# Performance work log

Measured on AMD Instinct MI355X. Metric: run time of the kernel, lower is better.

## Reference

```python
import math
import jax, jax.numpy as jnp
import numpy as np

D = 1024      # d_model
H = 16        # n_heads
HD = 64       # head_dim
DKV = D // 2  # 512
KVHD = DKV // H  # 32
HID = D // 8  # 128 (tau/delta hidden)
B, L, F = 2, 2048, 32


def setup_inputs() -> dict:
    key = jax.random.key(0)
    ks = jax.random.split(key, 16)
    s = 0.02
    return {
        "h": jax.random.normal(ks[0], (B, L, D), jnp.float32),
        "pre_norm_mu": jax.random.normal(ks[1], (B, L, F), jnp.float32),
        "pre_norm_sigma": jax.random.uniform(ks[2], (B, L, F), jnp.float32),
        "Wq": jax.random.normal(ks[3], (D, D), jnp.float32) * s,
        "Wk": jax.random.normal(ks[4], (D, DKV), jnp.float32) * s,
        "Wv": jax.random.normal(ks[5], (D, DKV), jnp.float32) * s,
        "Wo": jax.random.normal(ks[6], (DKV, D), jnp.float32) * s,
        "bo": jnp.zeros((D,), jnp.float32),
        "tau_w1": jax.random.normal(ks[7], (D + 1, HID), jnp.float32) * s,
        "tau_b1": jnp.zeros((HID,), jnp.float32),
        "tau_w2": jax.random.normal(ks[8], (HID, 1), jnp.float32) * s,
        "tau_b2": jnp.zeros((1,), jnp.float32),
        "del_w1": jax.random.normal(ks[9], (D + 1, HID), jnp.float32) * s,
        "del_b1": jnp.zeros((HID,), jnp.float32),
        "del_w2": jax.random.normal(ks[10], (HID, DKV), jnp.float32) * s,
        "del_b2": jnp.zeros((DKV,), jnp.float32),
    }


def _mlp(x, w1, b1, w2, b2):
    # Linear -> exact GELU -> Linear (matches torch nn.GELU default)
    return jax.nn.gelu(x @ w1 + b1, approximate=False) @ w2 + b2


def reference(h, pre_norm_mu, pre_norm_sigma, Wq, Wk, Wv, Wo, bo,
              tau_w1, tau_b1, tau_w2, tau_b2, del_w1, del_b1, del_w2, del_b2):
    b, l, _ = h.shape
    sigma_mean = jnp.clip(pre_norm_sigma.mean(axis=-1, keepdims=True), 1e-6, None)  # (B,L,1)
    mu_mean = pre_norm_mu.mean(axis=-1, keepdims=True)                               # (B,L,1)

    tau = jnp.exp(jnp.clip(_mlp(jnp.concatenate([sigma_mean, h], -1),
                                tau_w1, tau_b1, tau_w2, tau_b2), -3.0, 3.0))  # (B,L,1)
    delta = jnp.clip(_mlp(jnp.concatenate([mu_mean, h], -1),
                          del_w1, del_b1, del_w2, del_b2), -5.0, 5.0)          # (B,L,DKV)

    Q = (h @ Wq).reshape(b, l, H, HD).transpose(0, 2, 1, 3)       # (B,H,L,HD)
    K = (h @ Wk).reshape(b, l, H, KVHD).transpose(0, 2, 1, 3)     # (B,H,L,KVHD)
    V = (h @ Wv).reshape(b, l, H, KVHD).transpose(0, 2, 1, 3)

    Qc = Q[..., :KVHD]                                            # (B,H,L,KVHD)
    logits = jnp.einsum('bhqd,bhkd->bhqk', Qc, K) / math.sqrt(KVHD)
    logits = tau[:, None] * logits                                # tau -> (B,1,L,1): per-query scale

    delta_r = delta.reshape(b, l, H, KVHD).transpose(0, 2, 1, 3)  # (B,H,L,KVHD)
    delta_last = delta_r[:, :, -1, :]                             # (B,H,KVHD)
    delta_bias = jnp.einsum('bhd,bhkd->bhk', delta_last, K)       # (B,H,L_k)
    logits = logits + delta_bias[:, :, None, :]

    logits = jnp.clip(logits, -50.0, 50.0)
    causal = jnp.triu(jnp.ones((l, l), bool), 1)
    logits = jnp.where(causal, -jnp.inf, logits)

    attn = jax.nn.softmax(logits, axis=-1)
    out = jnp.einsum('bhqk,bhkd->bhqd', attn, V)                  # (B,H,L,KVHD)
    out = out.transpose(0, 2, 1, 3).reshape(b, l, DKV)
    out = out @ Wo + bo
    return out[:, -1, :]                                          # (B,D)
```

## Files before the change

### kernel.cpp

```cpp
#include <hip/hip_runtime.h>
#include <hip/hip_bf16.h>

#define Dm   1024
#define Hh   16
#define HDq  64
#define DKV  512
#define HID  128
#define Bb   2
#define Ll   2048
#define Ff   32

typedef _Float16 half8 __attribute__((ext_vector_type(8)));
typedef float f32x4 __attribute__((ext_vector_type(4)));

__device__ __forceinline__ float gelu_exact(float x) {
    return 0.5f * x * (1.0f + erff(x * 0.70710678118654752f));
}

__global__ __launch_bounds__(256) void kpart(
        const float* __restrict__ h, const float* __restrict__ Wq,
        const float* __restrict__ tw1, const float* __restrict__ dw1,
        float* __restrict__ hid_part, float* __restrict__ qc_part)
{
    const int bx = blockIdx.x, t = threadIdx.x;
    __shared__ float hl[128];
    __shared__ float red[256];
    if (bx < 32) {
        const int id = bx;
        const int b = (id >> 4) & 1, which = (id >> 3) & 1, jsplit = id & 7;
        const float* w1 = which ? dw1 : tw1;
        const float* hrow = h + ((size_t)b * Ll + (Ll - 1)) * Dm + jsplit * 128;
        if (t < 128) hl[t] = hrow[t];
        __syncthreads();
        const int col = t & 127, rg = t >> 7;
        const float* w1p = w1 + (size_t)(jsplit * 128 + rg + 1) * HID + col;
        float acc = 0.f;
#pragma unroll 8
        for (int p = 0; p < 64; ++p)
            acc += hl[p * 2 + rg] * w1p[(size_t)p * 2 * HID];
        red[t] = acc;
        __syncthreads();
        if (t < 128)
            hid_part[(((size_t)(b * 2 + which)) * 8 + jsplit) * HID + t] = red[t] + red[t + 128];
    } else {
        const int id = bx - 32;
        const int b = id >> 3, jsplit = id & 7;
        const float* hrow = h + ((size_t)b * Ll + (Ll - 1)) * Dm + jsplit * 128;
        if (t < 128) hl[t] = hrow[t];
        __syncthreads();
        const int c0 = t, c1 = t + 256;
        const int colq0 = (c0 >> 5) * HDq + (c0 & 31);
        const int colq1 = (c1 >> 5) * HDq + (c1 & 31);
        const float* Wq0 = Wq + (size_t)(jsplit * 128) * Dm;
        float a0 = 0.f, a1 = 0.f;
#pragma unroll 8
        for (int j = 0; j < 128; ++j) {
            const float x = hl[j];
            a0 += x * Wq0[(size_t)j * Dm + colq0];
            a1 += x * Wq0[(size_t)j * Dm + colq1];
        }
        float* qp = qc_part + ((size_t)b * 8 + jsplit) * DKV;
        qp[c0] = a0;
        qp[c1] = a1;
    }
}

__global__ __launch_bounds__(256) void kwcomb(
        const float* __restrict__ mu, const float* __restrict__ sigma,
        const float* __restrict__ tw1, const float* __restrict__ tb1,
        const float* __restrict__ tw2, const float* __restrict__ tb2,
        const float* __restrict__ dw1, const float* __restrict__ db1,
        const float* __restrict__ dw2, const float* __restrict__ db2,
        const float* __restrict__ hid_part, const float* __restrict__ qc_part,
        float* __restrict__ w_comb)
{
    const int cs = blockIdx.x, b = blockIdx.y;
    const int t = threadIdx.x;
    __shared__ float gh[HID];
    __shared__ float red[256];
    __shared__ float s_tau, s_sm, s_mm;

    if (t == 0) {
        float s = 0.f;
        for (int f = 0; f < Ff; ++f) s += sigma[((size_t)b * Ll + (Ll - 1)) * Ff + f];
        s_sm = fmaxf(s / (float)Ff, 1e-6f);
    }
    if (t == 64) {
        float s = 0.f;
        for (int f = 0; f < Ff; ++f) s += mu[((size_t)b * Ll + (Ll - 1)) * Ff + f];
        s_mm = s / (float)Ff;
    }
    __syncthreads();

    if (t < 128) {
        float a = tb1[t] + s_sm * tw1[t];
#pragma unroll
        for (int s = 0; s < 8; ++s)
            a += hid_part[(((size_t)(b * 2 + 0)) * 8 + s) * HID + t];
        red[t] = gelu_exact(a) * tw2[t];
    } else {
        const int hh = t - 128;
        float a = db1[hh] + s_mm * dw1[hh];
#pragma unroll
        for (int s = 0; s < 8; ++s)
            a += hid_part[(((size_t)(b * 2 + 1)) * 8 + s) * HID + hh];
        gh[hh] = gelu_exact(a);
        red[t] = 0.f;
    }
    __syncthreads();
    for (int s = 128; s > 0; s >>= 1) {
        if (t < s) red[t] += red[t + s];
        __syncthreads();
    }
    if (t == 0) {
        float s = red[0] + tb2[0];
        s_tau = expf(fminf(fmaxf(s, -3.f), 3.f));
    }
    __syncthreads();

    const int cl = t & 63, ih = t >> 6;
    const int c = cs * 64 + cl;
    float dacc = 0.f;
#pragma unroll 8
    for (int i = ih * 32; i < ih * 32 + 32; ++i)
        dacc += gh[i] * dw2[(size_t)i * DKV + c];
    red[t] = dacc;
    __syncthreads();
    if (t < 64) {
        const int cc = cs * 64 + t;
        float d = red[t] + red[t + 64] + red[t + 128] + red[t + 192] + db2[cc];
        d = fminf(fmaxf(d, -5.f), 5.f);
        float q = 0.f;
#pragma unroll
        for (int s = 0; s < 8; ++s)
            q += qc_part[((size_t)b * 8 + s) * DKV + cc];
        w_comb[(size_t)b * DKV + cc] = s_tau * q * 0.17677669529663687f + d;
    }
}

__global__ __launch_bounds__(256) void kkw(
        const float* __restrict__ Wk, const float* __restrict__ w_comb,
        _Float16* __restrict__ kwh16)
{
    const int jt = blockIdx.x, b = blockIdx.y;
    const int t = threadIdx.x;
    __shared__ float wc[DKV];
    __shared__ float kl[16][36];
    {
        float2 v = *(const float2*)(w_comb + (size_t)b * DKV + t * 2);
        wc[t * 2] = v.x; wc[t * 2 + 1] = v.y;
    }
    __syncthreads();
    const int c0 = t * 2;
    const float w0 = wc[c0], w1 = wc[c0 + 1];
    const int hd = t >> 4;
#pragma unroll 4
    for (int jj = 0; jj < 32; ++jj) {
        const int j = jt * 32 + jj;
        float2 kv = *(const float2*)(Wk + (size_t)j * DKV + c0);
        float p = kv.x * w0 + kv.y * w1;
        p += __shfl_xor(p, 1); p += __shfl_xor(p, 2);
        p += __shfl_xor(p, 4); p += __shfl_xor(p, 8);
        if ((t & 15) == 0) kl[hd][jj] = p;
    }
    __syncthreads();
    if (t < 64) {
        const int head = t & 15, jl = (t >> 4) * 8;
        half8 v;
#pragma unroll
        for (int e = 0; e < 8; ++e) v[e] = (_Float16)kl[head][jl + e];
        *(half8*)(kwh16 + ((size_t)(b * 32 + jt)) * 512 + t * 8) = v;
    }
}

__global__ __launch_bounds__(256) void klogit(
        const float* __restrict__ h, const _Float16* __restrict__ kwh16,
        float* __restrict__ p_arr, float* __restrict__ den_part)
{
    __shared__ __align__(16) _Float16 Kw[16384];
    __shared__ float lred[4][16][16];
    __shared__ float pden[16][16];
    const int bx = blockIdx.x, t = threadIdx.x;
    const int w = t >> 6, l = t & 63;
    const int rows0 = bx * 16, b = bx >> 7;

#pragma unroll
    for (int i = 0; i < 8; ++i) {
        const int idx = i * 256 + t;
        *(half8*)(Kw + idx * 8) = *(const half8*)(kwh16 + (size_t)b * 16384 + idx * 8);
    }
    __syncthreads();

    f32x4 lacc = {};
    const float* ap = h + (size_t)(rows0 + (l & 15)) * Dm + (l >> 4) * 8;
#pragma unroll
    for (int kk = 0; kk < 8; ++kk) {
        const int kt = w * 8 + kk;
        float4 x0 = *(const float4*)(ap + kt * 32);
        float4 x1 = *(const float4*)(ap + kt * 32 + 4);
        half8 af;
        af[0] = (_Float16)x0.x; af[1] = (_Float16)x0.y; af[2] = (_Float16)x0.z; af[3] = (_Float16)x0.w;
        af[4] = (_Float16)x1.x; af[5] = (_Float16)x1.y; af[6] = (_Float16)x1.z; af[7] = (_Float16)x1.w;
        half8 kf = *(const half8*)(Kw + kt * 512 + l * 8);
        lacc = __builtin_amdgcn_mfma_f32_16x16x32_f16(af, kf, lacc, 0, 0, 0);
    }
#pragma unroll
    for (int r = 0; r < 4; ++r)
        lred[w][(l >> 4) * 4 + r][l & 15] = lacc[r];
    __syncthreads();

    const int row16 = t >> 4, head = t & 15;
    float val = lred[0][row16][head] + lred[1][row16][head]
              + lred[2][row16][head] + lred[3][row16][head];
    val = fminf(fmaxf(val, -50.f), 50.f);
    const float e = __expf(val - 50.f);
    p_arr[(size_t)(rows0 + row16) * 16 + head] = e;
    pden[row16][head] = e;
    __syncthreads();
    if (t < 16) {
        float s = 0.f;
#pragma unroll
        for (int r = 0; r < 16; ++r) s += pden[r][t];
        den_part[((size_t)b * 16 + t) * 128 + (bx & 127)] = s;
    }
}

__global__ __launch_bounds__(256) void khbar(
        const float* __restrict__ hmat, const float* __restrict__ p_arr,
        float* __restrict__ hbar_part)
{
    const int jt = blockIdx.x, ls = blockIdx.y, b = blockIdx.z;
    const int t = threadIdx.x;
    __shared__ float P[2048];
#pragma unroll
    for (int i = 0; i < 2; ++i) {
        const int idx = i * 256 + t;
        *(float4*)(P + idx * 4) =
            *(const float4*)(p_arr + ((size_t)(b * Ll + ls * 128)) * 16 + idx * 4);
    }
    __syncthreads();
    const int hd = t & 15, jq = t >> 4;
    const float* hp = hmat + ((size_t)(b * Ll + ls * 128)) * Dm + jt * 128 + jq * 8;
    float4 a0 = {0.f, 0.f, 0.f, 0.f}, a1 = {0.f, 0.f, 0.f, 0.f};
#pragma unroll 4
    for (int l = 0; l < 128; ++l) {
        const float p = P[l * 16 + hd];
        float4 v0 = *(const float4*)(hp + (size_t)l * Dm);
        float4 v1 = *(const float4*)(hp + (size_t)l * Dm + 4);
        a0.x += p * v0.x; a0.y += p * v0.y; a0.z += p * v0.z; a0.w += p * v0.w;
        a1.x += p * v1.x; a1.y += p * v1.y; a1.z += p * v1.z; a1.w += p * v1.w;
    }
    float* dst = hbar_part + (((size_t)(b * 16 + hd)) * 16 + ls) * Dm + jt * 128 + jq * 8;
    *(float4*)dst = a0;
    *(float4*)(dst + 4) = a1;
}

__global__ __launch_bounds__(256) void kopre(
        const float* __restrict__ hbar_part, const float* __restrict__ den_part,
        const float* __restrict__ Wv, float* __restrict__ opre)
{
    const int hd = blockIdx.x, b = blockIdx.y;
    const int t = threadIdx.x;
    __shared__ float hb[Dm];
    __shared__ float4 red4[256];
    __shared__ float dred[128];
    __shared__ float s_den;

    if (t < 128) dred[t] = den_part[((size_t)b * 16 + hd) * 128 + t];
    float4 a = {0.f, 0.f, 0.f, 0.f};
#pragma unroll
    for (int ls = 0; ls < 16; ++ls) {
        float4 v = *(const float4*)(hbar_part + (((size_t)(b * 16 + hd)) * 16 + ls) * Dm + t * 4);
        a.x += v.x; a.y += v.y; a.z += v.z; a.w += v.w;
    }
    *(float4*)(hb + t * 4) = a;
    __syncthreads();
    if (t < 64) dred[t] += dred[t + 64];
    __syncthreads();
    if (t < 32) dred[t] += dred[t + 32];
    __syncthreads();
    if (t == 0) {
        float s = 0.f;
        for (int i = 0; i < 32; ++i) s += dred[i];
        s_den = s;
    }
    __syncthreads();

    const int d4 = (t & 7) * 4, jq = t >> 3;
    float4 acc = {0.f, 0.f, 0.f, 0.f};
#pragma unroll 8
    for (int j = jq * 32; j < jq * 32 + 32; ++j) {
        const float x = hb[j];
        float4 wv = *(const float4*)(Wv + (size_t)j * DKV + hd * 32 + d4);
        acc.x += x * wv.x; acc.y += x * wv.y; acc.z += x * wv.z; acc.w += x * wv.w;
    }
    red4[t] = acc;
    __syncthreads();
    if (t < 8) {
        float4 s = {0.f, 0.f, 0.f, 0.f};
#pragma unroll
        for (int g = 0; g < 32; ++g) {
            float4 v = red4[g * 8 + t];
            s.x += v.x; s.y += v.y; s.z += v.z; s.w += v.w;
        }
        const float inv = 1.0f / s_den;
        s.x *= inv; s.y *= inv; s.z *= inv; s.w *= inv;
        *(float4*)(opre + ((size_t)b * Hh + hd) * 32 + t * 4) = s;
    }
}

__global__ __launch_bounds__(256) void kout(
        const float* __restrict__ opre, const float* __restrict__ Wo,
        const float* __restrict__ bo, float* __restrict__ out)
{
    const int nt = blockIdx.x, b = blockIdx.y;
    const int t = threadIdx.x;
    __shared__ float op[DKV];
    __shared__ float red[256];
    if (t < 128)
        *(float4*)(op + t * 4) = *(const float4*)(opre + (size_t)b * DKV + t * 4);
    __syncthreads();
    const int nl = t & 63, cg = t >> 6;
    const int n = nt * 64 + nl;
    float acc = 0.f;
#pragma unroll 8
    for (int c = cg * 128; c < cg * 128 + 128; ++c)
        acc += op[c] * Wo[(size_t)c * Dm + n];
    red[t] = acc;
    __syncthreads();
    if (t < 64)
        out[(size_t)b * Dm + n] = bo[n] + red[t] + red[t + 64] + red[t + 128] + red[t + 192];
}

extern "C" void kernel_launch(void* const* d_in, const int* in_sizes, int n_in,
                              void* d_out, int out_size, void* d_ws, size_t ws_size,
                              hipStream_t stream) {
    const float* h      = (const float*)d_in[0];
    const float* mu     = (const float*)d_in[1];
    const float* sigma  = (const float*)d_in[2];
    const float* Wq     = (const float*)d_in[3];
    const float* Wk     = (const float*)d_in[4];
    const float* Wv     = (const float*)d_in[5];
    const float* Wo     = (const float*)d_in[6];
    const float* bo     = (const float*)d_in[7];
    const float* tau_w1 = (const float*)d_in[8];
    const float* tau_b1 = (const float*)d_in[9];
    const float* tau_w2 = (const float*)d_in[10];
    const float* tau_b2 = (const float*)d_in[11];
    const float* del_w1 = (const float*)d_in[12];
    const float* del_b1 = (const float*)d_in[13];
    const float* del_w2 = (const float*)d_in[14];
    const float* del_b2 = (const float*)d_in[15];
    float* out = (float*)d_out;

    _Float16* kwh16  = (_Float16*)d_ws;
    float* p_arr     = (float*)(kwh16 + 32768);
    float* den_part  = p_arr + 65536;
    float* hid_part  = den_part + 4096;
    float* qc_part   = hid_part + 4096;
    float* w_comb    = qc_part + 8192;
    float* hbar_part = w_comb + 1024;
    float* opre      = hbar_part + 524288;

    kpart<<<48, 256, 0, stream>>>(h, Wq, tau_w1, del_w1, hid_part, qc_part);
    kwcomb<<<dim3(8, Bb), 256, 0, stream>>>(mu, sigma, tau_w1, tau_b1, tau_w2, tau_b2,
                                            del_w1, del_b1, del_w2, del_b2,
                                            hid_part, qc_part, w_comb);
    kkw<<<dim3(32, Bb), 256, 0, stream>>>(Wk, w_comb, kwh16);
    klogit<<<256, 256, 0, stream>>>(h, kwh16, p_arr, den_part);
    khbar<<<dim3(8, 16, Bb), 256, 0, stream>>>(h, p_arr, hbar_part);
    kopre<<<dim3(16, Bb), 256, 0, stream>>>(hbar_part, den_part, Wv, opre);
    kout<<<dim3(16, Bb), 256, 0, stream>>>(opre, Wo, bo, out);
}
```

Measured before the change: 62.88 us.

## Fuse kernel chain: merge wcomb into kkw and logits into hbar accumulation

Merges the delta/tau combine kernel into the Wk projection kernel, so each of the 64 blocks recomputes the small MLP tail redundantly instead of paying a separate launch. It also fuses the logit/exp kernel with the weighted h-sum kernel using 32-row tiles, which keeps probabilities in LDS and drops the p_arr global round-trip, and it vectorises the Wq load in kpart. Risks: the redundant MLP work across blocks, only 128 blocks in the fused mid kernel, and h being read twice within a block.

```diff
diff --git a/kernel.cpp b/kernel.cpp
--- a/kernel.cpp
+++ b/kernel.cpp
@@ -48,36 +48,39 @@
         const float* hrow = h + ((size_t)b * Ll + (Ll - 1)) * Dm + jsplit * 128;
         if (t < 128) hl[t] = hrow[t];
         __syncthreads();
-        const int c0 = t, c1 = t + 256;
-        const int colq0 = (c0 >> 5) * HDq + (c0 & 31);
-        const int colq1 = (c1 >> 5) * HDq + (c1 & 31);
-        const float* Wq0 = Wq + (size_t)(jsplit * 128) * Dm;
-        float a0 = 0.f, a1 = 0.f;
+        float4 acc = {0.f, 0.f, 0.f, 0.f};
+        const float* Wq0 = Wq + (size_t)(jsplit * 128) * Dm + t * 4;
 #pragma unroll 8
         for (int j = 0; j < 128; ++j) {
             const float x = hl[j];
-            a0 += x * Wq0[(size_t)j * Dm + colq0];
-            a1 += x * Wq0[(size_t)j * Dm + colq1];
+            float4 wq = *(const float4*)(Wq0 + (size_t)j * Dm);
+            acc.x += x * wq.x; acc.y += x * wq.y;
+            acc.z += x * wq.z; acc.w += x * wq.w;
         }
-        float* qp = qc_part + ((size_t)b * 8 + jsplit) * DKV;
-        qp[c0] = a0;
-        qp[c1] = a1;
-    }
-}
-
-__global__ __launch_bounds__(256) void kwcomb(
+        const int col = t * 4;
+        if ((col & 63) < 32) {
+            const int c = (col >> 6) * 32 + (col & 31);
+            *(float4*)(qc_part + ((size_t)b * 8 + jsplit) * DKV + c) = acc;
+        }
+    }
+}
+
+__global__ __launch_bounds__(256) void kkw2(
         const float* __restrict__ mu, const float* __restrict__ sigma,
         const float* __restrict__ tw1, const float* __restrict__ tb1,
         const float* __restrict__ tw2, const float* __restrict__ tb2,
         const float* __restrict__ dw1, const float* __restrict__ db1,
         const float* __restrict__ dw2, const float* __restrict__ db2,
+        const float* __restrict__ Wk,
         const float* __restrict__ hid_part, const float* __restrict__ qc_part,
-        float* __restrict__ w_comb)
-{
-    const int cs = blockIdx.x, b = blockIdx.y;
+        _Float16* __restrict__ kwh16)
+{
+    const int jt = blockIdx.x, b = blockIdx.y;
     const int t = threadIdx.x;
     __shared__ float gh[HID];
     __shared__ float red[256];
+    __shared__ float wc[DKV];
+    __shared__ float kl[16][36];
     __shared__ float s_tau, s_sm, s_mm;
 
     if (t == 0) {
@@ -118,46 +121,34 @@
     }
     __syncthreads();
 
-    const int cl = t & 63, ih = t >> 6;
-    const int c = cs * 64 + cl;
-    float dacc = 0.f;
-#pragma unroll 8
-    for (int i = ih * 32; i < ih * 32 + 32; ++i)
-        dacc += gh[i] * dw2[(size_t)i * DKV + c];
-    red[t] = dacc;
-    __syncthreads();
-    if (t < 64) {
-        const int cc = cs * 64 + t;
-        float d = red[t] + red[t + 64] + red[t + 128] + red[t + 192] + db2[cc];
-        d = fminf(fmaxf(d, -5.f), 5.f);
-        float q = 0.f;
-#pragma unroll
-        for (int s = 0; s < 8; ++s)
-            q += qc_part[((size_t)b * 8 + s) * DKV + cc];
-        w_comb[(size_t)b * DKV + cc] = s_tau * q * 0.17677669529663687f + d;
-    }
-}
-
-__global__ __launch_bounds__(256) void kkw(
-        const float* __restrict__ Wk, const float* __restrict__ w_comb,
-        _Float16* __restrict__ kwh16)
-{
-    const int jt = blockIdx.x, b = blockIdx.y;
-    const int t = threadIdx.x;
-    __shared__ float wc[DKV];
-    __shared__ float kl[16][36];
-    {
-        float2 v = *(const float2*)(w_comb + (size_t)b * DKV + t * 2);
-        wc[t * 2] = v.x; wc[t * 2 + 1] = v.y;
-    }
-    __syncthreads();
-    const int c0 = t * 2;
-    const float w0 = wc[c0], w1 = wc[c0 + 1];
+    const int c0 = t, c1 = t + 256;
+    float d0 = db2[c0], d1 = db2[c1];
+#pragma unroll 8
+    for (int i = 0; i < HID; ++i) {
+        const float x = gh[i];
+        d0 += x * dw2[(size_t)i * DKV + c0];
+        d1 += x * dw2[(size_t)i * DKV + c1];
+    }
+    d0 = fminf(fmaxf(d0, -5.f), 5.f);
+    d1 = fminf(fmaxf(d1, -5.f), 5.f);
+    float q0 = 0.f, q1 = 0.f;
+#pragma unroll
+    for (int s = 0; s < 8; ++s) {
+        const float* qp = qc_part + ((size_t)b * 8 + s) * DKV;
+        q0 += qp[c0];
+        q1 += qp[c1];
+    }
+    const float inv_sqrt = 0.17677669529663687f;
+    wc[c0] = s_tau * q0 * inv_sqrt + d0;
+    wc[c1] = s_tau * q1 * inv_sqrt + d1;
+    __syncthreads();
+
+    const float w0 = wc[t * 2], w1 = wc[t * 2 + 1];
     const int hd = t >> 4;
 #pragma unroll 4
     for (int jj = 0; jj < 32; ++jj) {
         const int j = jt * 32 + jj;
-        float2 kv = *(const float2*)(Wk + (size_t)j * DKV + c0);
+        float2 kv = *(const float2*)(Wk + (size_t)j * DKV + t * 2);
         float p = kv.x * w0 + kv.y * w1;
         p += __shfl_xor(p, 1); p += __shfl_xor(p, 2);
         p += __shfl_xor(p, 4); p += __shfl_xor(p, 8);
@@ -173,16 +164,17 @@
     }
 }
 
-__global__ __launch_bounds__(256) void klogit(
+__global__ __launch_bounds__(256) void kmid(
         const float* __restrict__ h, const _Float16* __restrict__ kwh16,
-        float* __restrict__ p_arr, float* __restrict__ den_part)
+        float* __restrict__ den_part, float* __restrict__ hbar_part)
 {
     __shared__ __align__(16) _Float16 Kw[16384];
-    __shared__ float lred[4][16][16];
-    __shared__ float pden[16][16];
-    const int bx = blockIdx.x, t = threadIdx.x;
+    __shared__ float lred[4][32][17];
+    __shared__ float p_lds[32][16];
+    const int rt = blockIdx.x, b = blockIdx.y;
+    const int t = threadIdx.x;
     const int w = t >> 6, l = t & 63;
-    const int rows0 = bx * 16, b = bx >> 7;
+    const int rows0 = (b * 64 + rt) * 32;
 
 #pragma unroll
     for (int i = 0; i < 8; ++i) {
@@ -191,68 +183,69 @@
     }
     __syncthreads();
 
-    f32x4 lacc = {};
+    f32x4 lacc[2] = {};
     const float* ap = h + (size_t)(rows0 + (l & 15)) * Dm + (l >> 4) * 8;
 #pragma unroll
-    for (int kk = 0; kk < 8; ++kk) {
-        const int kt = w * 8 + kk;
-        float4 x0 = *(const float4*)(ap + kt * 32);
-        float4 x1 = *(const float4*)(ap + kt * 32 + 4);
-        half8 af;
-        af[0] = (_Float16)x0.x; af[1] = (_Float16)x0.y; af[2] = (_Float16)x0.z; af[3] = (_Float16)x0.w;
-        af[4] = (_Float16)x1.x; af[5] = (_Float16)x1.y; af[6] = (_Float16)x1.z; af[7] = (_Float16)x1.w;
-        half8 kf = *(const half8*)(Kw + kt * 512 + l * 8);
-        lacc = __builtin_amdgcn_mfma_f32_16x16x32_f16(af, kf, lacc, 0, 0, 0);
-    }
-#pragma unroll
-    for (int r = 0; r < 4; ++r)
-        lred[w][(l >> 4) * 4 + r][l & 15] = lacc[r];
-    __syncthreads();
-
-    const int row16 = t >> 4, head = t & 15;
-    float val = lred[0][row16][head] + lred[1][row16][head]
-              + lred[2][row16][head] + lred[3][row16][head];
-    val = fminf(fmaxf(val, -50.f), 50.f);
-    const float e = __expf(val - 50.f);
-    p_arr[(size_t)(rows0 + row16) * 16 + head] = e;
-    pden[row16][head] = e;
-    __syncthreads();
+    for (int mt = 0; mt < 2; ++mt) {
+        const float* apm = ap + (size_t)mt * 16 * Dm;
+#pragma unroll
+        for (int ks = 0; ks < 8; ++ks) {
+            const int kt = w * 8 + ks;
+            float4 x0 = *(const float4*)(apm + kt * 32);
+            float4 x1 = *(const float4*)(apm + kt * 32 + 4);
+            half8 af;
+            af[0] = (_Float16)x0.x; af[1] = (_Float16)x0.y; af[2] = (_Float16)x0.z; af[3] = (_Float16)x0.w;
+            af[4] = (_Float16)x1.x; af[5] = (_Float16)x1.y; af[6] = (_Float16)x1.z; af[7] = (_Float16)x1.w;
+            half8 kf = *(const half8*)(Kw + kt * 512 + l * 8);
+            lacc[mt] = __builtin_amdgcn_mfma_f32_16x16x32_f16(af, kf, lacc[mt], 0, 0, 0);
+        }
+    }
+#pragma unroll
+    for (int mt = 0; mt < 2; ++mt)
+#pragma unroll
+        for (int r = 0; r < 4; ++r)
+            lred[w][mt * 16 + (l >> 4) * 4 + r][l & 15] = lacc[mt][r];
+    __syncthreads();
+
+#pragma unroll
+    for (int i = 0; i < 2; ++i) {
+        const int row = i * 16 + (t >> 4), head = t & 15;
+        float val = lred[0][row][head] + lred[1][row][head]
+                  + lred[2][row][head] + lred[3][row][head];
+        val = fminf(fmaxf(val, -50.f), 50.f);
+        p_lds[row][head] = __expf(val - 50.f);
+    }
+    __syncthreads();
+
     if (t < 16) {
         float s = 0.f;
 #pragma unroll
-        for (int r = 0; r < 16; ++r) s += pden[r][t];
-        den_part[((size_t)b * 16 + t) * 128 + (bx & 127)] = s;
-    }
-}
-
-__global__ __launch_bounds__(256) void khbar(
-        const float* __restrict__ hmat, const float* __restrict__ p_arr,
-        float* __restrict__ hbar_part)
-{
-    const int jt = blockIdx.x, ls = blockIdx.y, b = blockIdx.z;
-    const int t = threadIdx.x;
-    __shared__ float P[2048];
-#pragma unroll
-    for (int i = 0; i < 2; ++i) {
-        const int idx = i * 256 + t;
-        *(float4*)(P + idx * 4) =
-            *(const float4*)(p_arr + ((size_t)(b * Ll + ls * 128)) * 16 + idx * 4);
-    }
-    __syncthreads();
-    const int hd = t & 15, jq = t >> 4;
-    const float* hp = hmat + ((size_t)(b * Ll + ls * 128)) * Dm + jt * 128 + jq * 8;
-    float4 a0 = {0.f, 0.f, 0.f, 0.f}, a1 = {0.f, 0.f, 0.f, 0.f};
-#pragma unroll 4
-    for (int l = 0; l < 128; ++l) {
-        const float p = P[l * 16 + hd];
-        float4 v0 = *(const float4*)(hp + (size_t)l * Dm);
-        float4 v1 = *(const float4*)(hp + (size_t)l * Dm + 4);
-        a0.x += p * v0.x; a0.y += p * v0.y; a0.z += p * v0.z; a0.w += p * v0.w;
-        a1.x += p * v1.x; a1.y += p * v1.y; a1.z += p * v1.z; a1.w += p * v1.w;
-    }
-    float* dst = hbar_part + (((size_t)(b * 16 + hd)) * 16 + ls) * Dm + jt * 128 + jq * 8;
-    *(float4*)dst = a0;
-    *(float4*)(dst + 4) = a1;
+        for (int r = 0; r < 32; ++r) s += p_lds[r][t];
+        den_part[((size_t)b * Hh + t) * 64 + rt] = s;
+    }
+
+    const int j0 = (t & 63) * 16;
+    const int h0 = (t >> 6) * 4;
+    f32x4 acc[4][4] = {};
+    for (int l2 = 0; l2 < 32; ++l2) {
+        const float* hr = h + (size_t)(rows0 + l2) * Dm + j0;
+        f32x4 hv[4];
+#pragma unroll
+        for (int jj = 0; jj < 4; ++jj) hv[jj] = *(const f32x4*)(hr + jj * 4);
+        f32x4 pp = *(const f32x4*)(&p_lds[l2][h0]);
+#pragma unroll
+        for (int hh = 0; hh < 4; ++hh)
+#pragma unroll
+            for (int jj = 0; jj < 4; ++jj)
+                acc[jj][hh] += hv[jj] * pp[hh];
+    }
+#pragma unroll
+    for (int hh = 0; hh < 4; ++hh) {
+        float* dst = hbar_part + (((size_t)(b * 64 + rt)) * Hh + h0 + hh) * Dm + j0;
+#pragma unroll
+        for (int jj = 0; jj < 4; ++jj)
+            *(f32x4*)(dst + jj * 4) = acc[jj][hh];
+    }
 }
 
 __global__ __launch_bounds__(256) void kopre(
@@ -262,20 +255,16 @@
     const int hd = blockIdx.x, b = blockIdx.y;
     const int t = threadIdx.x;
     __shared__ float hb[Dm];
-    __shared__ float4 red4[256];
-    __shared__ float dred[128];
+    __shared__ float red[256];
+    __shared__ float dred[64];
     __shared__ float s_den;
 
-    if (t < 128) dred[t] = den_part[((size_t)b * 16 + hd) * 128 + t];
-    float4 a = {0.f, 0.f, 0.f, 0.f};
-#pragma unroll
-    for (int ls = 0; ls < 16; ++ls) {
-        float4 v = *(const float4*)(hbar_part + (((size_t)(b * 16 + hd)) * 16 + ls) * Dm + t * 4);
-        a.x += v.x; a.y += v.y; a.z += v.z; a.w += v.w;
-    }
-    *(float4*)(hb + t * 4) = a;
-    __syncthreads();
-    if (t < 64) dred[t] += dred[t + 64];
+    if (t >= 192) dred[t - 192] = den_part[((size_t)b * Hh + hd) * 64 + (t - 192)];
+    f32x4 a = {};
+#pragma unroll 8
+    for (int rt = 0; rt < 64; ++rt)
+        a += *(const f32x4*)(hbar_part + (((size_t)(b * 64 + rt)) * Hh + hd) * Dm + t * 4);
+    *(f32x4*)(hb + t * 4) = a;
     __syncthreads();
     if (t < 32) dred[t] += dred[t + 32];
     __syncthreads();
@@ -286,26 +275,19 @@
     }
     __syncthreads();
 
-    const int d4 = (t & 7) * 4, jq = t >> 3;
-    float4 acc = {0.f, 0.f, 0.f, 0.f};
-#pragma unroll 8
-    for (int j = jq * 32; j < jq * 32 + 32; ++j) {
-        const float x = hb[j];
-        float4 wv = *(const float4*)(Wv + (size_t)j * DKV + hd * 32 + d4);
-        acc.x += x * wv.x; acc.y += x * wv.y; acc.z += x * wv.z; acc.w += x * wv.w;
-    }
-    red4[t] = acc;
-    __syncthreads();
-    if (t < 8) {
-        float4 s = {0.f, 0.f, 0.f, 0.f};
-#pragma unroll
-        for (int g = 0; g < 32; ++g) {
-            float4 v = red4[g * 8 + t];
-            s.x += v.x; s.y += v.y; s.z += v.z; s.w += v.w;
-        }
-        const float inv = 1.0f / s_den;
-        s.x *= inv; s.y *= inv; s.z *= inv; s.w *= inv;
-        *(float4*)(opre + ((size_t)b * Hh + hd) * 32 + t * 4) = s;
+    const int c = hd * 32 + (t & 31);
+    float accv = 0.f;
+    const int jbase = (t >> 5) * 128;
+#pragma unroll 8
+    for (int j = jbase; j < jbase + 128; ++j)
+        accv += hb[j] * Wv[(size_t)j * DKV + c];
+    red[t] = accv;
+    __syncthreads();
+    if (t < 32) {
+        float s = 0.f;
+#pragma unroll
+        for (int g = 0; g < 8; ++g) s += red[g * 32 + t];
+        opre[((size_t)b * Hh + hd) * 32 + t] = s / s_den;
     }
 }
 
@@ -354,21 +336,17 @@
     float* out = (float*)d_out;
 
     _Float16* kwh16  = (_Float16*)d_ws;
-    float* p_arr     = (float*)(kwh16 + 32768);
-    float* den_part  = p_arr + 65536;
-    float* hid_part  = den_part + 4096;
+    float* den_part  = (float*)(kwh16 + 32768);
+    float* hid_part  = den_part + 2048;
     float* qc_part   = hid_part + 4096;
-    float* w_comb    = qc_part + 8192;
-    float* hbar_part = w_comb + 1024;
-    float* opre      = hbar_part + 524288;
+    float* opre      = qc_part + 8192;
+    float* hbar_part = opre + 1024;
 
     kpart<<<48, 256, 0, stream>>>(h, Wq, tau_w1, del_w1, hid_part, qc_part);
-    kwcomb<<<dim3(8, Bb), 256, 0, stream>>>(mu, sigma, tau_w1, tau_b1, tau_w2, tau_b2,
-                                            del_w1, del_b1, del_w2, del_b2,
-                                            hid_part, qc_part, w_comb);
-    kkw<<<dim3(32, Bb), 256, 0, stream>>>(Wk, w_comb, kwh16);
-    klogit<<<256, 256, 0, stream>>>(h, kwh16, p_arr, den_part);
-    khbar<<<dim3(8, 16, Bb), 256, 0, stream>>>(h, p_arr, hbar_part);
+    kkw2<<<dim3(32, Bb), 256, 0, stream>>>(mu, sigma, tau_w1, tau_b1, tau_w2, tau_b2,
+                                           del_w1, del_b1, del_w2, del_b2, Wk,
+                                           hid_part, qc_part, kwh16);
+    kmid<<<dim3(64, Bb), 256, 0, stream>>>(h, kwh16, den_part, hbar_part);
     kopre<<<dim3(16, Bb), 256, 0, stream>>>(hbar_part, den_part, Wv, opre);
     kout<<<dim3(16, Bb), 256, 0, stream>>>(opre, Wo, bo, out);
 }
```

Measured after the change: 67.16 us. 1.07x slower.
